# Performance work log

Measured on AMD Instinct MI355X. Metric: run time of the kernel, lower is better.

Reference implementation:

```python
import jax, jax.numpy as jnp
import numpy as np

N, D, C, T = 4096, 1024, 1000, 32  # tokens, n_embd, n_class, n_logit_samples


def setup_inputs() -> dict:
    key = jax.random.key(0)
    k1, k2 = jax.random.split(key)
    x = jax.random.normal(k1, (N, D), dtype=jnp.float32)
    # 0.02 init scale keeps exp(logvar) numerically sane (standard GPT-style init)
    W = jax.random.normal(k2, (2 * C, D), dtype=jnp.float32) * 0.02
    return {"x": x, "W": W}


def reference(x, W):
    # linear head (bias-free): [N, D] @ [D, 2C] -> [N, 2C]
    h = jnp.einsum('nd,cd->nc', x, W)
    mu, logvar = h[:, :C], h[:, C:]
    sigma = jnp.exp(0.5 * logvar)  # sqrt(exp(logvar))

    # MC sampling of logits, vectorized over the T sample loop.
    # torch subtracts the row max before softmax; that is exactly what a
    # numerically-stable softmax does, so the math is identical.
    eps = jax.random.normal(jax.random.key(42), (T, N, C), dtype=mu.dtype)
    logits = mu[None] + sigma[None] * eps           # [T, N, C]
    probs = jax.nn.softmax(logits, axis=-1)         # [T, N, C]
    prob = jnp.mean(probs, axis=0)                  # [N, C]
    mu_out = jnp.exp(prob)                          # faithful to torch.exp(prob)
    return (mu_out, sigma)
```

## Files before the change

### kernel.cpp

```cpp
#include <hip/hip_runtime.h>


typedef __attribute__((ext_vector_type(8))) _Float16 f16x8;
typedef __attribute__((ext_vector_type(4))) float f32x4;
typedef __attribute__((ext_vector_type(2))) float f32x2;

#define NC_TOT  4096000
#define H_HALF  65536000u

__device__ __forceinline__ unsigned short f2h(float f) {
  _Float16 h = (_Float16)f;
  return __builtin_bit_cast(unsigned short, h);
}

__global__ __launch_bounds__(256) void convert_kernel(
    const float* __restrict__ x, const float* __restrict__ W,
    unsigned short* __restrict__ xh, unsigned short* __restrict__ wh) {
  int qid = blockIdx.x * 256 + threadIdx.x;
  if (qid < 1048576) {
    float4 v = ((const float4*)x)[qid];
    ((ushort4*)xh)[qid] = make_ushort4(f2h(v.x), f2h(v.y), f2h(v.z), f2h(v.w));
  } else {
    int q = qid - 1048576;
    int row = q >> 8;
    ushort4 o;
    if (row < 2000) {
      float4 v = ((const float4*)W)[q];
      o = make_ushort4(f2h(v.x), f2h(v.y), f2h(v.z), f2h(v.w));
    } else {
      o = make_ushort4(0, 0, 0, 0);
    }
    ((ushort4*)wh)[q] = o;
  }
}

#define BK 32

typedef __attribute__((address_space(3))) unsigned char lds_byte;
typedef __attribute__((address_space(1))) unsigned char glb_byte;

__device__ __forceinline__ void glds16(const unsigned short* g, unsigned short* l) {
  __builtin_amdgcn_global_load_lds((const glb_byte*)g, (lds_byte*)l, 16, 0, 0);
}

__global__ __launch_bounds__(256) void gemm_kernel(
    const unsigned short* __restrict__ Ah,
    const unsigned short* __restrict__ Bh,
    float* __restrict__ mu,
    float* __restrict__ sigma_out) {
  const int K = 1024;
  __shared__ unsigned short As[128 * BK];
  __shared__ unsigned short Bs[64 * BK];

  int id  = blockIdx.x;
  int xcd = id & 7;
  int q9  = id >> 3;
  int by  = xcd * 4 + (q9 >> 5);
  int bx  = q9 & 31;

  int tid  = threadIdx.x;
  int w    = tid >> 6;
  int lane = tid & 63;
  int wr   = (w >> 1) * 64;
  int wc   = (w & 1) * 32;
  int lrow = lane & 15;
  int kq   = lane >> 4;

  f32x4 acc[4][2];
  for (int i = 0; i < 4; i++)
    for (int j = 0; j < 2; j++) acc[i][j] = (f32x4){0.f, 0.f, 0.f, 0.f};

  int srow = w * 16 + (lane >> 2);
  int scol = (lane & 3) * 8;
  const unsigned short* Ap = Ah + (by * 128 + srow) * K + scol;
  const unsigned short* Bp = Bh + (bx * 64  + srow) * K + scol;
  unsigned short* lA = As + w * 512;
  unsigned short* lB = Bs + w * 512;

  for (int kk = 0; kk < K; kk += BK) {
    __syncthreads();
    glds16(Ap + kk,          lA);
    glds16(Ap + kk + 64 * K, lA + 2048);
    glds16(Bp + kk,          lB);
    __syncthreads();

    f16x8 a[4], b[2];
    for (int i = 0; i < 4; i++)
      a[i] = *(const f16x8*)(As + (wr + i * 16 + lrow) * BK + kq * 8);
    for (int j = 0; j < 2; j++)
      b[j] = *(const f16x8*)(Bs + (wc + j * 16 + lrow) * BK + kq * 8);
    for (int i = 0; i < 4; i++)
      for (int j = 0; j < 2; j++)
        acc[i][j] = __builtin_amdgcn_mfma_f32_16x16x32_f16(a[i], b[j], acc[i][j], 0, 0, 0);
  }

  int orow0 = by * 128 + wr + (lane >> 4) * 4;
  int ocol0 = bx * 64 + wc + (lane & 15);
  for (int i = 0; i < 4; i++) {
    for (int j = 0; j < 2; j++) {
      int c = ocol0 + j * 16;
      for (int v = 0; v < 4; v++) {
        int r = orow0 + i * 16 + v;
        float val = acc[i][j][v];
        if (c < 1000)       mu[r * 1000 + c] = val;
        else if (c < 2000)  sigma_out[r * 1000 + (c - 1000)] = __expf(0.5f * val);
      }
    }
  }
}

__device__ __forceinline__ void threefry(unsigned x0, unsigned x1,
                                         unsigned& o0, unsigned& o1) {
  const unsigned ks1 = 42u;
  const unsigned ks2 = 0x1BD11BDAu ^ 42u;
#define TF_RND(r) { x0 += x1; x1 = (x1 << (r)) | (x1 >> (32 - (r))); x1 ^= x0; }
  x1 += ks1;
  TF_RND(13) TF_RND(15) TF_RND(26) TF_RND(6)
  x0 += ks1;  x1 += ks2 + 1u;
  TF_RND(17) TF_RND(29) TF_RND(16) TF_RND(24)
  x0 += ks2;  x1 += 2u;
  TF_RND(13) TF_RND(15) TF_RND(26) TF_RND(6)
  x1 += ks1 + 3u;
  TF_RND(17) TF_RND(29) TF_RND(16) TF_RND(24)
  x0 += ks1;  x1 += ks2 + 4u;
  TF_RND(13) TF_RND(15) TF_RND(26) TF_RND(6)
  x0 += ks2;  x1 += 5u;
#undef TF_RND
  o0 = x0; o1 = x1;
}

__device__ __forceinline__ float erfinv_big(float x, float w) {
  float v = __fsqrt_rn(w) - 3.0f;
  float p = -0.000200214257f;
  p = fmaf(p, v, 0.000100950558f);
  p = fmaf(p, v, 0.00134934322f);
  p = fmaf(p, v, -0.00367342844f);
  p = fmaf(p, v, 0.00573950773f);
  p = fmaf(p, v, -0.0076224613f);
  p = fmaf(p, v, 0.00943887047f);
  p = fmaf(p, v, 1.00167406f);
  p = fmaf(p, v, 2.83297682f);
  return 1.41421356f * (p * x);
}

__device__ __forceinline__ f32x2 splat2(float c) { return (f32x2){c, c}; }

__device__ __forceinline__ f32x2 normal2(f32x2 x) {
  f32x2 t = __builtin_elementwise_fma(-x, x, splat2(1.0f));
  f32x2 lg;
  lg.x = __builtin_amdgcn_logf(t.x);
  lg.y = __builtin_amdgcn_logf(t.y);
  f32x2 w = lg * splat2(-0.69314718f);
  f32x2 v = w - splat2(2.5f);
  f32x2 p = splat2(2.81022636e-08f);
  p = __builtin_elementwise_fma(p, v, splat2(3.43273939e-07f));
  p = __builtin_elementwise_fma(p, v, splat2(-3.5233877e-06f));
  p = __builtin_elementwise_fma(p, v, splat2(-4.39150654e-06f));
  p = __builtin_elementwise_fma(p, v, splat2(0.00021858087f));
  p = __builtin_elementwise_fma(p, v, splat2(-0.00125372503f));
  p = __builtin_elementwise_fma(p, v, splat2(-0.00417768164f));
  p = __builtin_elementwise_fma(p, v, splat2(0.246640727f));
  p = __builtin_elementwise_fma(p, v, splat2(1.50140941f));
  f32x2 r = (p * x) * splat2(1.41421356f);
  if (w.x >= 5.0f) r.x = erfinv_big(x.x, w.x);
  if (w.y >= 5.0f) r.y = erfinv_big(x.y, w.y);
  return r;
}

__device__ __forceinline__ f32x2 bits_to_u2(unsigned b0, unsigned b1) {
  f32x2 f;
  f.x = __builtin_bit_cast(float, (b0 >> 9) | 0x3f800000u);
  f.y = __builtin_bit_cast(float, (b1 >> 9) | 0x3f800000u);
  f = f - splat2(1.0f);
  return __builtin_elementwise_fma(f, splat2(2.0f), splat2(-0.99999994f));
}

__global__ __launch_bounds__(256) void sample_kernel(
    const float* __restrict__ mu,
    const float* __restrict__ sigma,
    float* __restrict__ out0) {
  int n    = blockIdx.x;
  int tid  = threadIdx.x;
  int lane = tid & 63, w = tid >> 6;
  __shared__ float pbuf[4][1024];

  int cb = n * 1000;
  float muv[16], sgv[16], prob[16];
#pragma unroll
  for (int j = 0; j < 16; j++) {
    int c = j * 64 + lane;
    bool val = (c < 1000);
    muv[j] = val ? mu[cb + c]    : 0.f;
    sgv[j] = val ? sigma[cb + c] : 0.f;
    prob[j] = 0.f;
  }

  f32x2 e[16];
#pragma unroll 1
  for (int it = 0; it < 4; it++) {
    int t = w * 4 + it;
    unsigned ib = (unsigned)(t * 4096000 + cb) + (unsigned)lane;
    f32x2 s = splat2(0.f);
#pragma unroll
    for (int j = 0; j < 16; j++) {
      unsigned i0 = ib + (unsigned)(j * 64);
      unsigned o0, o1;
      threefry(i0, i0 + H_HALF, o0, o1);
      f32x2 eps = normal2(bits_to_u2(o0, o1));
      f32x2 lg = __builtin_elementwise_fma(splat2(sgv[j]), eps, splat2(muv[j]));
      f32x2 ev;
      ev.x = __expf(lg.x);
      ev.y = __expf(lg.y);
      if (j == 15) {
        ev.x = (lane < 40) ? ev.x : 0.f;
        ev.y = (lane < 40) ? ev.y : 0.f;
      }
      e[j] = ev;
      s = s + ev;
    }
#pragma unroll
    for (int m = 1; m < 64; m <<= 1) {
      s.x += __shfl_xor(s.x, m, 64);
      s.y += __shfl_xor(s.y, m, 64);
    }
    float rA = 1.0f / s.x, rB = 1.0f / s.y;
#pragma unroll
    for (int j = 0; j < 16; j++)
      prob[j] = fmaf(e[j].x, rA, fmaf(e[j].y, rB, prob[j]));
  }

#pragma unroll
  for (int j = 0; j < 16; j++)
    pbuf[w][j * 64 + lane] = prob[j];
  __syncthreads();
#pragma unroll
  for (int k = 0; k < 4; k++) {
    int c = tid + k * 256;
    if (c < 1000) {
      float sm = pbuf[0][c] + pbuf[1][c] + pbuf[2][c] + pbuf[3][c];
      out0[cb + c] = __expf(sm * 0.03125f);
    }
  }
}

extern "C" void kernel_launch(void* const* d_in, const int* in_sizes, int n_in,
                              void* d_out, int out_size, void* d_ws, size_t ws_size,
                              hipStream_t stream) {
  const float* x = (const float*)d_in[0];
  const float* W = (const float*)d_in[1];
  float* out = (float*)d_out;

  unsigned short* xh = (unsigned short*)d_ws;
  unsigned short* wh = (unsigned short*)((char*)d_ws + 8388608);
  float*          mu = (float*)((char*)d_ws + 12582912);
  float* sigma = out + NC_TOT;

  convert_kernel<<<6144, 256, 0, stream>>>(x, W, xh, wh);
  gemm_kernel<<<1024, 256, 0, stream>>>(xh, wh, mu, sigma);
  sample_kernel<<<4096, 256, 0, stream>>>(mu, sigma, out);
}
```

Measured before the change: 294.5 us.

## Split sample rows across wave pairs and fold constants into exp2 arithmetic

The sample kernel now gives each pair of waves half of the class columns for 8 sample draws, instead of one wave per 4 samples covering all 1000 columns. This cuts per-thread register arrays from 16 to 8 and removes the masked tail lane. Row sums are combined through LDS with a barrier each iteration. Scale factors (log2e, sqrt2) are folded into mu/sigma so exp2 and rcp intrinsics replace expf and division. Threefry rotates use alignbit, and the erfinv branch test works on the log directly. The added per-iteration __syncthreads could cost latency in exchange for better occupancy.

```diff
diff --git a/kernel.cpp b/kernel.cpp
--- a/kernel.cpp
+++ b/kernel.cpp
@@ -109,11 +109,15 @@
   }
 }
 
+__device__ __forceinline__ unsigned rotl_(unsigned x, unsigned r) {
+  return __builtin_amdgcn_alignbit(x, x, 32u - r);
+}
+
 __device__ __forceinline__ void threefry(unsigned x0, unsigned x1,
                                          unsigned& o0, unsigned& o1) {
   const unsigned ks1 = 42u;
   const unsigned ks2 = 0x1BD11BDAu ^ 42u;
-#define TF_RND(r) { x0 += x1; x1 = (x1 << (r)) | (x1 >> (32 - (r))); x1 ^= x0; }
+#define TF_RND(r) { x0 += x1; x1 = rotl_(x1, r); x1 ^= x0; }
   x1 += ks1;
   TF_RND(13) TF_RND(15) TF_RND(26) TF_RND(6)
   x0 += ks1;  x1 += ks2 + 1u;
@@ -129,7 +133,10 @@
   o0 = x0; o1 = x1;
 }
 
-__device__ __forceinline__ float erfinv_big(float x, float w) {
+__device__ __forceinline__ f32x2 splat2(float c) { return (f32x2){c, c}; }
+
+__device__ __forceinline__ float erfinv_big_p(float x, float lg) {
+  float w = lg * -0.69314718f;
   float v = __fsqrt_rn(w) - 3.0f;
   float p = -0.000200214257f;
   p = fmaf(p, v, 0.000100950558f);
@@ -140,18 +147,15 @@
   p = fmaf(p, v, 0.00943887047f);
   p = fmaf(p, v, 1.00167406f);
   p = fmaf(p, v, 2.83297682f);
-  return 1.41421356f * (p * x);
-}
-
-__device__ __forceinline__ f32x2 splat2(float c) { return (f32x2){c, c}; }
-
-__device__ __forceinline__ f32x2 normal2(f32x2 x) {
+  return p * x;
+}
+
+__device__ __forceinline__ f32x2 normal2p(f32x2 x) {
   f32x2 t = __builtin_elementwise_fma(-x, x, splat2(1.0f));
   f32x2 lg;
   lg.x = __builtin_amdgcn_logf(t.x);
   lg.y = __builtin_amdgcn_logf(t.y);
-  f32x2 w = lg * splat2(-0.69314718f);
-  f32x2 v = w - splat2(2.5f);
+  f32x2 v = __builtin_elementwise_fma(lg, splat2(-0.69314718f), splat2(-2.5f));
   f32x2 p = splat2(2.81022636e-08f);
   p = __builtin_elementwise_fma(p, v, splat2(3.43273939e-07f));
   p = __builtin_elementwise_fma(p, v, splat2(-3.5233877e-06f));
@@ -161,9 +165,9 @@
   p = __builtin_elementwise_fma(p, v, splat2(-0.00417768164f));
   p = __builtin_elementwise_fma(p, v, splat2(0.246640727f));
   p = __builtin_elementwise_fma(p, v, splat2(1.50140941f));
-  f32x2 r = (p * x) * splat2(1.41421356f);
-  if (w.x >= 5.0f) r.x = erfinv_big(x.x, w.x);
-  if (w.y >= 5.0f) r.y = erfinv_big(x.y, w.y);
+  f32x2 r = p * x;
+  if (lg.x <= -7.2134752f) r.x = erfinv_big_p(x.x, lg.x);
+  if (lg.y <= -7.2134752f) r.y = erfinv_big_p(x.y, lg.y);
   return r;
 }
 
@@ -181,40 +185,44 @@
     float* __restrict__ out0) {
   int n    = blockIdx.x;
   int tid  = threadIdx.x;
-  int lane = tid & 63, w = tid >> 6;
-  __shared__ float pbuf[4][1024];
-
-  int cb = n * 1000;
-  float muv[16], sgv[16], prob[16];
-#pragma unroll
-  for (int j = 0; j < 16; j++) {
-    int c = j * 64 + lane;
+  int lane = tid & 63;
+  int w    = tid >> 6;
+  int half = w & 1;
+  int tg   = w >> 1;
+  __shared__ float pbuf[2][1024];
+  __shared__ f32x2 sred[2][2][2];
+
+  int cb    = n * 1000;
+  int cbase = half * 512;
+
+  const float L2E    = 1.44269504f;
+  const float SQ2L2E = 1.41421356f * 1.44269504f;
+
+  float mu2[8], sg2[8], prob[8];
+#pragma unroll
+  for (int j = 0; j < 8; j++) {
+    int c = cbase + j * 64 + lane;
     bool val = (c < 1000);
-    muv[j] = val ? mu[cb + c]    : 0.f;
-    sgv[j] = val ? sigma[cb + c] : 0.f;
+    mu2[j]  = val ? mu[cb + c] * L2E       : -1e30f;
+    sg2[j]  = val ? sigma[cb + c] * SQ2L2E : 0.f;
     prob[j] = 0.f;
   }
 
-  f32x2 e[16];
+  f32x2 e[8];
 #pragma unroll 1
-  for (int it = 0; it < 4; it++) {
-    int t = w * 4 + it;
-    unsigned ib = (unsigned)(t * 4096000 + cb) + (unsigned)lane;
+  for (int it = 0; it < 8; it++) {
+    int t = tg * 8 + it;
+    unsigned ib = (unsigned)(t * 4096000 + cb + cbase) + (unsigned)lane;
     f32x2 s = splat2(0.f);
 #pragma unroll
-    for (int j = 0; j < 16; j++) {
+    for (int j = 0; j < 8; j++) {
       unsigned i0 = ib + (unsigned)(j * 64);
       unsigned o0, o1;
       threefry(i0, i0 + H_HALF, o0, o1);
-      f32x2 eps = normal2(bits_to_u2(o0, o1));
-      f32x2 lg = __builtin_elementwise_fma(splat2(sgv[j]), eps, splat2(muv[j]));
+      f32x2 epsp = normal2p(bits_to_u2(o0, o1));
       f32x2 ev;
-      ev.x = __expf(lg.x);
-      ev.y = __expf(lg.y);
-      if (j == 15) {
-        ev.x = (lane < 40) ? ev.x : 0.f;
-        ev.y = (lane < 40) ? ev.y : 0.f;
-      }
+      ev.x = __builtin_amdgcn_exp2f(fmaf(sg2[j], epsp.x, mu2[j]));
+      ev.y = __builtin_amdgcn_exp2f(fmaf(sg2[j], epsp.y, mu2[j]));
       e[j] = ev;
       s = s + ev;
     }
@@ -223,22 +231,27 @@
       s.x += __shfl_xor(s.x, m, 64);
       s.y += __shfl_xor(s.y, m, 64);
     }
-    float rA = 1.0f / s.x, rB = 1.0f / s.y;
-#pragma unroll
-    for (int j = 0; j < 16; j++)
+    if (lane == 0) sred[it & 1][tg][half] = s;
+    __syncthreads();
+    f32x2 s0 = sred[it & 1][tg][0];
+    f32x2 s1 = sred[it & 1][tg][1];
+    float rA = __builtin_amdgcn_rcpf(s0.x + s1.x);
+    float rB = __builtin_amdgcn_rcpf(s0.y + s1.y);
+#pragma unroll
+    for (int j = 0; j < 8; j++)
       prob[j] = fmaf(e[j].x, rA, fmaf(e[j].y, rB, prob[j]));
   }
 
 #pragma unroll
-  for (int j = 0; j < 16; j++)
-    pbuf[w][j * 64 + lane] = prob[j];
+  for (int j = 0; j < 8; j++)
+    pbuf[tg][cbase + j * 64 + lane] = prob[j];
   __syncthreads();
 #pragma unroll
   for (int k = 0; k < 4; k++) {
     int c = tid + k * 256;
     if (c < 1000) {
-      float sm = pbuf[0][c] + pbuf[1][c] + pbuf[2][c] + pbuf[3][c];
-      out0[cb + c] = __expf(sm * 0.03125f);
+      float sm = pbuf[0][c] + pbuf[1][c];
+      out0[cb + c] = __builtin_amdgcn_exp2f(sm * (0.03125f * 1.44269504f));
     }
   }
 }
```

Result: slower. 323.2 us (+9.7%).
